# Optimization experiments

Measured on AMD Instinct MI355X. Metric: run time of the kernel, lower is better.

The kernel has to match this reference:

```python
import jax, jax.numpy as jnp
import numpy as np

K = 12           # boundary_k
TEMP = 0.75      # logit_temperature


def _knn_idx(p):
    # p: [N,3]; brute-force kNN within one batch element (pointops offsets => per-batch)
    sq = jnp.sum(p * p, axis=-1)
    d2 = sq[:, None] + sq[None, :] - 2.0 * (p @ p.T)   # [N,N]
    _, idx = jax.lax.top_k(-d2, K + 1)                  # self is nearest (d=0)
    return idx[:, 1:]                                    # drop self -> [N,K]


def _mlp2(x, W1, b1, W2, b2, relu_out):
    h = jax.nn.relu(x @ W1 + b1) @ W2 + b2
    return jax.nn.relu(h) if relu_out else h


def setup_inputs() -> dict:
    key = jax.random.key(0)
    ks = jax.random.split(key, 32)
    B, N, C = 4, 4096, 17
    dims = [256, 512, 768]
    RD = 320
    s = 0.02
    inp = {
        'feat0': jax.random.normal(ks[0], (B, N, dims[0]), jnp.float32),
        'feat1': jax.random.normal(ks[1], (B, N, dims[1]), jnp.float32),
        'feat2': jax.random.normal(ks[2], (B, N, dims[2]), jnp.float32),
        'logits': jax.random.normal(ks[3], (B, N, C), jnp.float32),
        'labels': jax.random.randint(ks[4], (B, N), 0, C, jnp.int32),
        'pos': jax.random.normal(ks[5], (B, N, 3), jnp.float32),
    }
    # feat projections
    for i, d in enumerate(dims):
        inp[f'Wp{i}'] = jax.random.normal(ks[6 + i], (d, RD), jnp.float32) * s
        inp[f'bp{i}'] = jnp.zeros((RD,), jnp.float32)
    # boundary encoder 6->96->160
    inp['Wbe1'] = jax.random.normal(ks[10], (6, 96), jnp.float32) * s
    inp['bbe1'] = jnp.zeros((96,), jnp.float32)
    inp['Wbe2'] = jax.random.normal(ks[11], (96, 160), jnp.float32) * s
    inp['bbe2'] = jnp.zeros((160,), jnp.float32)
    # attention (RD+160)->320->n_scales
    inp['Wa1'] = jax.random.normal(ks[12], (RD + 160, 320), jnp.float32) * s
    inp['ba1'] = jnp.zeros((320,), jnp.float32)
    inp['Wa2'] = jax.random.normal(ks[13], (320, 3), jnp.float32) * s
    inp['ba2'] = jnp.zeros((3,), jnp.float32)
    # output proj RD->RD->RD
    inp['Wo1'] = jax.random.normal(ks[14], (RD, RD), jnp.float32) * s
    inp['bo1'] = jnp.zeros((RD,), jnp.float32)
    inp['Wo2'] = jax.random.normal(ks[15], (RD, RD), jnp.float32) * s
    inp['bo2'] = jnp.zeros((RD,), jnp.float32)
    return inp


def boundary_info(logits, labels, pos):
    idx = jax.vmap(_knn_idx)(pos)                          # [B,N,K]
    nb_lab = jax.vmap(lambda l, i: l[i])(labels, idx)      # [B,N,K]
    nb_pos = jax.vmap(lambda p, i: p[i])(pos, idx)         # [B,N,K,3]
    diff = nb_lab != labels[..., None]                     # [B,N,K]
    diff_f = diff.astype(jnp.float32)
    dist = jnp.linalg.norm(nb_pos - pos[:, :, None, :], axis=-1)  # [B,N,K]
    boundary_score = diff_f.mean(axis=-1)
    same = 1.0 - diff_f
    same_dist = (dist * same).sum(-1) / (same.sum(-1) + 1e-6)
    bdist = jnp.min(jnp.where(diff, dist, jnp.inf), axis=-1)
    bdist = jnp.where(jnp.isfinite(bdist), bdist, same_dist)
    mean_d = dist.mean(-1)
    density = 1.0 / (mean_d + 1e-6)
    curvature = jnp.std(dist, axis=-1, ddof=1) / (mean_d + 1e-6)  # torch.std unbiased
    probs = jax.nn.softmax(logits / TEMP, axis=-1)
    confidence = probs.max(-1)
    entropy = -(probs * jnp.log(probs + 1e-8)).sum(-1) / jnp.log(jnp.float32(probs.shape[-1]))
    return jnp.stack([boundary_score, confidence, entropy, density, curvature, bdist], axis=-1)


def reference(feat0, feat1, feat2, logits, labels, pos,
              Wp0, bp0, Wp1, bp1, Wp2, bp2,
              Wbe1, bbe1, Wbe2, bbe2,
              Wa1, ba1, Wa2, ba2,
              Wo1, bo1, Wo2, bo2):
    fp = jnp.stack([feat0 @ Wp0 + bp0, feat1 @ Wp1 + bp1, feat2 @ Wp2 + bp2], axis=2)  # [B,N,3,RD]
    info = boundary_info(logits, labels, pos)                       # [B,N,6]
    enc = _mlp2(info, Wbe1, bbe1, Wbe2, bbe2, relu_out=True)        # [B,N,160]
    global_feat = fp.mean(axis=2)                                   # [B,N,RD]
    attn_in = jnp.concatenate([global_feat, enc], axis=-1)
    attn = jax.nn.softmax(_mlp2(attn_in, Wa1, ba1, Wa2, ba2, relu_out=False), axis=-1)  # [B,N,3]
    fused = (fp * attn[..., None]).sum(axis=2)                      # [B,N,RD]
    out = _mlp2(fused, Wo1, bo1, Wo2, bo2, relu_out=False) + global_feat
    return out, attn
```

## Files before the change

kernel.cpp:

```cpp
#include <hip/hip_runtime.h>
#include <stdint.h>

typedef float fx4 __attribute__((ext_vector_type(4)));
typedef short s8 __attribute__((ext_vector_type(8)));
typedef short s4 __attribute__((ext_vector_type(4)));
typedef unsigned int u32;
typedef u32 ux4 __attribute__((ext_vector_type(4)));

#define MTOT 16384
#define NPTS 4096

#define VMCNT6 asm volatile("s_waitcnt vmcnt(6)" ::: "memory")
#define VMCNT4 asm volatile("s_waitcnt vmcnt(4)" ::: "memory")
#define VMCNT0 asm volatile("s_waitcnt vmcnt(0)" ::: "memory")
#define LGKM0  asm volatile("s_waitcnt lgkmcnt(0)" ::: "memory")
#define SBAR   asm volatile("s_barrier" ::: "memory")
#define SCHED0 __builtin_amdgcn_sched_barrier(0)

__device__ __forceinline__ float b2f(short s) {
    return __uint_as_float(((unsigned)(unsigned short)s) << 16);
}
__device__ __forceinline__ short f2b(float f) {
    unsigned u = __float_as_uint(f);
    u += 0x7fffu + ((u >> 16) & 1u);
    return (short)(u >> 16);
}
__device__ __forceinline__ void g2l16(const void* g, void* l) {
    __builtin_amdgcn_global_load_lds(
        (const __attribute__((address_space(1))) unsigned int*)g,
        (__attribute__((address_space(3))) unsigned int*)l, 16, 0, 0);
}
__device__ __forceinline__ void g2l4(const void* g, void* l) {
    __builtin_amdgcn_global_load_lds(
        (const __attribute__((address_space(1))) unsigned int*)g,
        (__attribute__((address_space(3))) unsigned int*)l, 4, 0, 0);
}

struct WTDesc {
    const float* W[8];
    short* Bt[8];
    int K[8];
    int N[8];
    int Kp[8];
    int swz[8];
    int base[9];
};

__global__ __launch_bounds__(256) void wtrans8_kernel(WTDesc d)
{
    int idx = blockIdx.x * 256 + threadIdx.x;
    if (idx >= d.base[8]) return;
    int s = 0;
#pragma unroll
    for (int t = 1; t < 8; ++t) if (idx >= d.base[t]) s = t;
    int local = idx - d.base[s];
    int N = d.N[s];
    if (d.swz[s]) {
        int c = local / 10240, r = local - c * 10240;
        int n = r >> 5, q = r & 31, slot = q >> 3, t = q & 7;
        int kl = ((slot ^ ((n >> 1) & 3)) << 3) | t;
        int k = c * 32 + kl;
        d.Bt[s][local] = f2b(d.W[s][(size_t)k * N + n]);
    } else {
        int Kp = d.Kp[s], K = d.K[s];
        int n = local / Kp, k = local - n * Kp;
        d.Bt[s][local] = (k < K) ? f2b(d.W[s][(size_t)k * N + n]) : (short)0;
    }
}

#define SEGW 132
#define KCAP 40

__global__ __launch_bounds__(512) void knap_kernel(
    const float* __restrict__ pos, u32* __restrict__ keys,
    const float* __restrict__ f0, const float* __restrict__ f1, const float* __restrict__ f2,
    short* __restrict__ a0, short* __restrict__ a1, short* __restrict__ a2)
{
    __shared__ float xs[8 * SEGW], ys[8 * SEGW], zs[8 * SEGW];
    __shared__ u32 cand[64 * KCAP];
    __shared__ u32 samp[64 * 16];
    __shared__ u32 tauA[64];
    __shared__ int cnt[64];

    if (blockIdx.x >= 1024) {
        int g = (blockIdx.x - 1024) * 512 + threadIdx.x;
        const float* src; short* dst; int K; size_t w;
        if (g < 1572864)      { src = f2; dst = a2; K = 768; w = (size_t)g * 8; }
        else if (g < 2621440) { src = f1; dst = a1; K = 512; w = (size_t)(g - 1572864) * 8; }
        else                  { src = f0; dst = a0; K = 256; w = (size_t)(g - 2621440) * 8; }
        int Kt = K * 64;
        int mtile = (int)(w / (size_t)Kt);
        int r2 = (int)(w - (size_t)mtile * Kt);
        int chunk = r2 >> 11;
        int within = r2 & 2047;
        int r = within >> 5, q = within & 31;
        int slot = q >> 3;
        int k = chunk * 32 + ((slot ^ ((r >> 1) & 3)) << 3);
        int row = mtile * 64 + r;
        const float* sp = src + (size_t)row * K + k;
        fx4 v0 = *(const fx4*)sp, v1 = *(const fx4*)(sp + 4);
        s8 o;
        o[0] = f2b(v0[0]); o[1] = f2b(v0[1]); o[2] = f2b(v0[2]); o[3] = f2b(v0[3]);
        o[4] = f2b(v1[0]); o[5] = f2b(v1[1]); o[6] = f2b(v1[2]); o[7] = f2b(v1[3]);
        *(s8*)(dst + w) = o;
        return;
    }

    int bid = blockIdx.x;
    int b   = bid >> 8;
    int cc  = (bid >> 6) & 3;
    int pch = bid & 63;
    int tid = threadIdx.x;
    int jb  = cc << 10;

    if (tid < 64) cnt[tid] = 0;
    for (int idx = tid; idx < 1024; idx += 512) {
        int seg = idx >> 7, o = idx & 127;
        const float* pp = pos + (size_t)(b * NPTS + jb + idx) * 3;
        xs[seg * SEGW + o] = pp[0];
        ys[seg * SEGW + o] = pp[1];
        zs[seg * SEGW + o] = pp[2];
    }
    __syncthreads();

    int lp = tid >> 3, q = tid & 7;
    int gi = pch * 64 + lp;
    const float* mp = pos + (size_t)(b * NPTS + gi) * 3;
    float mx = mp[0], my = mp[1], mz = mp[2];

    const float* xsq = xs + q * SEGW;
    const float* ysq = ys + q * SEGW;
    const float* zsq = zs + q * SEGW;
    int jg0 = jb + q * 128;

    u32 h0 = 0xFFFFFFFFu, h1v = 0xFFFFFFFFu;
    for (int jj = 0; jj < 128; jj += 4) {
        fx4 xv = *reinterpret_cast<const fx4*>(xsq + jj);
        fx4 yv = *reinterpret_cast<const fx4*>(ysq + jj);
        fx4 zv = *reinterpret_cast<const fx4*>(zsq + jj);
#pragma unroll
        for (int u = 0; u < 4; ++u) {
            float dx = xv[u] - mx, dy = yv[u] - my, dz = zv[u] - mz;
            float d2 = fmaf(dx, dx, fmaf(dy, dy, dz * dz));
            int jg = jg0 + jj + u;
            u32 key = (__float_as_uint(d2) & 0xFFFFF000u) | (u32)jg;
            if (jg == gi) key = 0xFFFFFFFFu;
            u32 lo = (key < h0) ? key : h0;
            u32 hi = (key < h0) ? h0 : key;
            h0 = lo;
            h1v = (hi < h1v) ? hi : h1v;
        }
    }
    samp[lp * 16 + q * 2]     = h0;
    samp[lp * 16 + q * 2 + 1] = h1v;
    __syncthreads();

    {
        ux4 sv0 = *(ux4*)&samp[lp * 16];
        ux4 sv1 = *(ux4*)&samp[lp * 16 + 4];
        ux4 sv2 = *(ux4*)&samp[lp * 16 + 8];
        ux4 sv3 = *(ux4*)&samp[lp * 16 + 12];
        int r0 = 0, r1 = 0;
#pragma unroll
        for (int i = 0; i < 4; ++i) {
            r0 += (sv0[i] < h0) + (sv1[i] < h0) + (sv2[i] < h0) + (sv3[i] < h0);
            r1 += (sv0[i] < h1v) + (sv1[i] < h1v) + (sv2[i] < h1v) + (sv3[i] < h1v);
        }
        if (r0 == 11) tauA[lp] = h0;
        if (r1 == 11) tauA[lp] = h1v;
    }
    __syncthreads();
    u32 tau = tauA[lp];

    for (int jj = 0; jj < 128; jj += 4) {
        fx4 xv = *reinterpret_cast<const fx4*>(xsq + jj);
        fx4 yv = *reinterpret_cast<const fx4*>(ysq + jj);
        fx4 zv = *reinterpret_cast<const fx4*>(zsq + jj);
#pragma unroll
        for (int u = 0; u < 4; ++u) {
            float dx = xv[u] - mx, dy = yv[u] - my, dz = zv[u] - mz;
            float d2 = fmaf(dx, dx, fmaf(dy, dy, dz * dz));
            int jg = jg0 + jj + u;
            u32 key = (__float_as_uint(d2) & 0xFFFFF000u) | (u32)jg;
            if (jg == gi) key = 0xFFFFFFFFu;
            if (key <= tau) {
                int slot = atomicAdd(&cnt[lp], 1);
                if (slot < KCAP) cand[lp * KCAP + slot] = key;
            }
        }
    }
    __syncthreads();

    int n = cnt[lp];
    u32 out[12];
    if (n <= KCAP) {
        u32 e0, e1, e2, e3, e4;
        e0 = (q      < n) ? cand[lp * KCAP + q]      : 0xFFFFFFFFu;
        e1 = (q + 8  < n) ? cand[lp * KCAP + q + 8]  : 0xFFFFFFFFu;
        e2 = (q + 16 < n) ? cand[lp * KCAP + q + 16] : 0xFFFFFFFFu;
        e3 = (q + 24 < n) ? cand[lp * KCAP + q + 24] : 0xFFFFFFFFu;
        e4 = (q + 32 < n) ? cand[lp * KCAP + q + 32] : 0xFFFFFFFFu;
#define CE(a, b) { u32 t0 = (a < b) ? a : b; u32 t1 = (a < b) ? b : a; a = t0; b = t1; }
        CE(e0, e1) CE(e1, e2) CE(e2, e3) CE(e3, e4)
        CE(e0, e1) CE(e1, e2) CE(e2, e3)
        CE(e0, e1) CE(e1, e2)
        CE(e0, e1)
#undef CE
        cand[lp * KCAP + q]      = e0;
        cand[lp * KCAP + q + 8]  = e1;
        cand[lp * KCAP + q + 16] = e2;
        cand[lp * KCAP + q + 24] = e3;
        cand[lp * KCAP + q + 32] = e4;
        int ptr = 0;
        u32 head = e0;
#pragma unroll
        for (int r = 0; r < 12; ++r) {
            u32 m = head;
            u32 o1 = __shfl_xor(m, 4, 8); m = (o1 < m) ? o1 : m;
            u32 o2 = __shfl_xor(m, 2, 8); m = (o2 < m) ? o2 : m;
            u32 o3 = __shfl_xor(m, 1, 8); m = (o3 < m) ? o3 : m;
            if (m == head) {
                ++ptr;
                head = (ptr < 5) ? cand[lp * KCAP + q + ptr * 8] : 0xFFFFFFFFu;
            }
            out[r] = m;
        }
    } else {
        u32 hk[12];
#pragma unroll
        for (int k = 0; k < 12; ++k) hk[k] = 0xFFFFFFFFu;
        for (int jj = 0; jj < 128; jj += 4) {
            fx4 xv = *reinterpret_cast<const fx4*>(xsq + jj);
            fx4 yv = *reinterpret_cast<const fx4*>(ysq + jj);
            fx4 zv = *reinterpret_cast<const fx4*>(zsq + jj);
#pragma unroll
            for (int u = 0; u < 4; ++u) {
                float dx = xv[u] - mx, dy = yv[u] - my, dz = zv[u] - mz;
                float d2 = fmaf(dx, dx, fmaf(dy, dy, dz * dz));
                int jg = jg0 + jj + u;
                u32 key = (__float_as_uint(d2) & 0xFFFFF000u) | (u32)jg;
                if (jg == gi) key = 0xFFFFFFFFu;
                if (key < hk[11]) {
                    hk[11] = key;
#pragma unroll
                    for (int k = 11; k >= 1; --k) {
                        u32 a = hk[k], bb = hk[k - 1];
                        u32 mn = (a < bb) ? a : bb;
                        u32 mxv = (a < bb) ? bb : a;
                        hk[k - 1] = mn; hk[k] = mxv;
                    }
                }
            }
        }
#pragma unroll
        for (int r = 0; r < 12; ++r) {
            u32 m = hk[0];
            u32 o1 = __shfl_xor(m, 4, 8); m = (o1 < m) ? o1 : m;
            u32 o2 = __shfl_xor(m, 2, 8); m = (o2 < m) ? o2 : m;
            u32 o3 = __shfl_xor(m, 1, 8); m = (o3 < m) ? o3 : m;
            if (m == hk[0]) {
#pragma unroll
                for (int k = 0; k < 11; ++k) hk[k] = hk[k + 1];
                hk[11] = 0xFFFFFFFFu;
            }
            out[r] = m;
        }
    }

    size_t kb = ((size_t)(b * NPTS + gi) * 4 + cc) * 12;
    if (q == 0) *reinterpret_cast<ux4*>(&keys[kb])     = (ux4){out[0], out[1], out[2], out[3]};
    if (q == 1) *reinterpret_cast<ux4*>(&keys[kb + 4]) = (ux4){out[4], out[5], out[6], out[7]};
    if (q == 2) *reinterpret_cast<ux4*>(&keys[kb + 8]) = (ux4){out[8], out[9], out[10], out[11]};
}

__global__ __launch_bounds__(256) void knn_merge_kernel(
    const u32* __restrict__ keys, const int* __restrict__ labels,
    const float* __restrict__ logits, float* __restrict__ info32)
{
    __shared__ unsigned char labs[NPTS];
    int b  = blockIdx.x >> 6;
    int pc = blockIdx.x & 63;
    int tid = threadIdx.x;
    for (int idx = tid; idx < NPTS; idx += 256)
        labs[idx] = (unsigned char)labels[b * NPTS + idx];
    __syncthreads();

    int lp = tid >> 2, q = tid & 3;
    int gi = pc * 64 + lp;
    size_t kb = ((size_t)(b * NPTS + gi) * 4 + q) * 12;
    ux4 k0 = *reinterpret_cast<const ux4*>(&keys[kb]);
    ux4 k1 = *reinterpret_cast<const ux4*>(&keys[kb + 4]);
    ux4 k2 = *reinterpret_cast<const ux4*>(&keys[kb + 8]);
    u32 hk[12];
    hk[0] = k0[0]; hk[1] = k0[1]; hk[2] = k0[2]; hk[3] = k0[3];
    hk[4] = k1[0]; hk[5] = k1[1]; hk[6] = k1[2]; hk[7] = k1[3];
    hk[8] = k2[0]; hk[9] = k2[1]; hk[10] = k2[2]; hk[11] = k2[3];

    int mylab = (int)labs[gi];
    float sum_d = 0.f, sum_d2 = 0.f, sum_diff = 0.f, same_d = 0.f, bmin = 3.0e38f;
#pragma unroll
    for (int r = 0; r < 12; ++r) {
        u32 m = hk[0];
        u32 o1 = __shfl_xor(m, 2, 4); m = (o1 < m) ? o1 : m;
        u32 o2 = __shfl_xor(m, 1, 4); m = (o2 < m) ? o2 : m;
        if (m == hk[0]) {
#pragma unroll
            for (int k = 0; k < 11; ++k) hk[k] = hk[k + 1];
            hk[11] = 0xFFFFFFFFu;
        }
        float d = sqrtf(__uint_as_float(m & 0xFFFFF000u));
        int j = (int)(m & 0xFFFu);
        float isdiff = ((int)labs[j] != mylab) ? 1.0f : 0.0f;
        sum_d += d;
        sum_d2 = fmaf(d, d, sum_d2);
        sum_diff += isdiff;
        same_d = fmaf(d, 1.0f - isdiff, same_d);
        if (isdiff > 0.f) bmin = fminf(bmin, d);
    }

    if (q == 0) {
        float nsame = 12.0f - sum_diff;
        float mean_d = sum_d * (1.0f / 12.0f);
        float var = fmaxf(0.f, (sum_d2 - 12.0f * mean_d * mean_d) * (1.0f / 11.0f));
        float md_eps = mean_d + 1e-6f;
        float curvature = sqrtf(var) / md_eps;
        float density = 1.0f / md_eps;
        float same_dist = same_d / (nsame + 1e-6f);
        float bdist = (bmin < 2.9e38f) ? bmin : same_dist;
        float bscore = sum_diff * (1.0f / 12.0f);

        const float* lg = logits + (size_t)(b * NPTS + gi) * 17;
        float v[17];
        float vmax = -3.0e38f;
#pragma unroll
        for (int c = 0; c < 17; ++c) { v[c] = lg[c] * (1.0f / 0.75f); vmax = fmaxf(vmax, v[c]); }
        float ssum = 0.f;
#pragma unroll
        for (int c = 0; c < 17; ++c) { v[c] = expf(v[c] - vmax); ssum += v[c]; }
        float inv = 1.0f / ssum;
        float conf = 0.f, ent = 0.f;
#pragma unroll
        for (int c = 0; c < 17; ++c) {
            float pprob = v[c] * inv;
            conf = fmaxf(conf, pprob);
            ent += pprob * logf(pprob + 1e-8f);
        }
        ent = -ent * (1.0f / 2.8332133f);

        float* op = info32 + (size_t)(b * NPTS + gi) * 32;
        fx4 o0 = {bscore, conf, ent, density};
        fx4 o1v = {curvature, bdist, 0.f, 0.f};
        fx4 zz = {0.f, 0.f, 0.f, 0.f};
        *reinterpret_cast<fx4*>(op + 0)  = o0;
        *reinterpret_cast<fx4*>(op + 4)  = o1v;
        *reinterpret_cast<fx4*>(op + 8)  = zz;
        *reinterpret_cast<fx4*>(op + 12) = zz;
        *reinterpret_cast<fx4*>(op + 16) = zz;
        *reinterpret_cast<fx4*>(op + 20) = zz;
        *reinterpret_cast<fx4*>(op + 24) = zz;
        *reinterpret_cast<fx4*>(op + 28) = zz;
    }
}

template<bool AF32, bool RELU, bool NMASK, bool ADDF, bool OUTF, bool OUTB>
__global__ __launch_bounds__(256) void gemm_k(
    const void* __restrict__ Ap, int lda,
    const short* __restrict__ Bt,
    const float* __restrict__ bias,
    float* __restrict__ Cf, int ldcf,
    short* __restrict__ Cb, int ldcb, int cboff,
    const float* __restrict__ Af, int ldaf,
    int N, int K, int ntiles)
{
    __shared__ short As[128 * 40];
    __shared__ short Bs[64 * 40];
    int bid = blockIdx.x;
    int mt = bid / ntiles, nt = bid - mt * ntiles;
    int m0 = mt * 128, n0 = nt * 64;
    int tid = threadIdx.x, l = tid & 63, wid = tid >> 6;
    int wm = wid & 1, wn = wid >> 1, lr = l & 15, lh = l >> 4;
    fx4 acc[4][2] = {};

    int nsteps = K >> 5;
    for (int kt = 0; kt < nsteps; ++kt) {
        int k0 = kt << 5;
        if constexpr (AF32) {
            const float* A = (const float*)Ap;
#pragma unroll
            for (int it = 0; it < 4; ++it) {
                int tt = tid + it * 256;
                int row = tt >> 3, seg = tt & 7;
                fx4 vv = *reinterpret_cast<const fx4*>(A + (size_t)(m0 + row) * lda + k0 + seg * 4);
                s4 w; w[0] = f2b(vv[0]); w[1] = f2b(vv[1]); w[2] = f2b(vv[2]); w[3] = f2b(vv[3]);
                *reinterpret_cast<s4*>(&As[row * 40 + seg * 4]) = w;
            }
        } else {
            const short* A = (const short*)Ap;
#pragma unroll
            for (int it = 0; it < 2; ++it) {
                int tt = tid + it * 256;
                int row = tt >> 2, seg = tt & 3;
                s8 vv = *reinterpret_cast<const s8*>(A + (size_t)(m0 + row) * lda + k0 + seg * 8);
                *reinterpret_cast<s8*>(&As[row * 40 + seg * 8]) = vv;
            }
        }
        {
            int row = tid >> 2, seg = tid & 3;
            s8 vb = {0, 0, 0, 0, 0, 0, 0, 0};
            if (!NMASK || (n0 + row) < N)
                vb = *reinterpret_cast<const s8*>(Bt + (size_t)(n0 + row) * K + k0 + seg * 8);
            *reinterpret_cast<s8*>(&Bs[row * 40 + seg * 8]) = vb;
        }
        __syncthreads();
        s8 af[4], bfr[2];
#pragma unroll
        for (int mf = 0; mf < 4; ++mf)
            af[mf] = *reinterpret_cast<s8*>(&As[(wm * 64 + mf * 16 + lr) * 40 + lh * 8]);
#pragma unroll
        for (int nf = 0; nf < 2; ++nf)
            bfr[nf] = *reinterpret_cast<s8*>(&Bs[(wn * 32 + nf * 16 + lr) * 40 + lh * 8]);
#pragma unroll
        for (int mf = 0; mf < 4; ++mf)
#pragma unroll
            for (int nf = 0; nf < 2; ++nf)
                acc[mf][nf] = __builtin_amdgcn_mfma_f32_16x16x32_bf16(af[mf], bfr[nf], acc[mf][nf], 0, 0, 0);
        __syncthreads();
    }

#pragma unroll
    for (int nf = 0; nf < 2; ++nf) {
        int col = n0 + wn * 32 + nf * 16 + lr;
        if (NMASK && col >= N) continue;
        float bv = bias[col];
#pragma unroll
        for (int mf = 0; mf < 4; ++mf) {
            int r0 = m0 + wm * 64 + mf * 16 + lh * 4;
#pragma unroll
            for (int rg = 0; rg < 4; ++rg) {
                float c = acc[mf][nf][rg] + bv;
                if (RELU) c = fmaxf(c, 0.0f);
                int row = r0 + rg;
                if constexpr (ADDF) c += Af[(size_t)row * ldaf + col];
                if constexpr (OUTF) Cf[(size_t)row * ldcf + col] = c;
                if constexpr (OUTB) Cb[(size_t)row * ldcb + cboff + col] = f2b(c);
            }
        }
    }
}

__global__ __launch_bounds__(512, 1) void mega_kernel(
    const short* __restrict__ at0, const short* __restrict__ at1, const short* __restrict__ at2,
    const short* __restrict__ btp0, const short* __restrict__ btp1, const short* __restrict__ btp2,
    const float* __restrict__ bp0, const float* __restrict__ bp1, const float* __restrict__ bp2,
    const short* __restrict__ bta1, const float* __restrict__ ba1,
    const float* __restrict__ Wa2, const float* __restrict__ ba2,
    const short* __restrict__ bto1, const float* __restrict__ bo1,
    const short* __restrict__ bto2, const float* __restrict__ bo2,
    const short* __restrict__ encb,
    float* __restrict__ outf, float* __restrict__ attn_out)
{
    __shared__ alignas(16) char smb[136192];
    const int BBo[3] = {0, 20480, 40960};
    const int ABo[3] = {61440, 65536, 69632};
    constexpr int R2B = 73728, SWF = 135168;
    float* smf = (float*)(smb + SWF);

    int tid = threadIdx.x, wid = tid >> 6, l = tid & 63;
    int wm = wid >> 2, wn = wid & 3, lr = l & 15, lh = l >> 4;
    int m0 = blockIdx.x * 64;

    auto stageB = [&](int bbase, const short* btg, int kt) {
        const char* s = (const char*)(btg + (size_t)kt * 10240);
        int o1 = wid * 1024 + l * 16;
        int o2 = 8192 + o1;
        int o3 = 16384 + wid * 256 + l * 4;
        int o4 = 2048 + o3;
        g2l16(s + o1, smb + bbase + o1);
        g2l16(s + o2, smb + bbase + o2);
        g2l4(s + o3, smb + bbase + o3);
        g2l4(s + o4, smb + bbase + o4);
    };
    auto stageA = [&](int abase, const short* atgm, int kt) {
        const char* s = (const char*)(atgm + (size_t)kt * 2048);
        int o1 = wid * 256 + l * 4;
        int o2 = 2048 + o1;
        g2l4(s + o1, smb + abase + o1);
        g2l4(s + o2, smb + abase + o2);
    };
    auto readB = [&](int bbase, s8* bf) {
#pragma unroll
        for (int nf = 0; nf < 5; ++nf) {
            int row = wn * 80 + nf * 16 + lr;
            bf[nf] = *(const s8*)(smb + bbase + row * 64 + ((lh ^ ((row >> 1) & 3)) << 4));
        }
    };
    auto readA = [&](int abase, s8* af) {
#pragma unroll
        for (int mf = 0; mf < 2; ++mf) {
            int row = wm * 32 + mf * 16 + lr;
            af[mf] = *(const s8*)(smb + abase + row * 64 + ((lh ^ ((row >> 1) & 3)) << 4));
        }
    };

    fx4 gacc[2][5] = {};

    auto do_proj = [&](const short* atgm, const short* btg, int ns,
                       const float* bias, s4 (&fpks)[2][5]) {
        fx4 acc[2][5] = {};
        stageB(BBo[0], btg, 0); stageA(ABo[0], atgm, 0);
        stageB(BBo[1], btg, 1); stageA(ABo[1], atgm, 1);
        LGKM0;
#pragma unroll 1
        for (int kt = 0; kt < ns; ++kt) {
            if (kt < ns - 1) { VMCNT6; } else { VMCNT0; }
            SBAR;
            int ph = kt - (kt / 3) * 3;
            s8 af[2], bf[5];
            readA(ABo[ph], af);
            readB(BBo[ph], bf);
            if (kt + 2 < ns) {
                int p2 = (kt + 2) - ((kt + 2) / 3) * 3;
                stageB(BBo[p2], btg, kt + 2);
                stageA(ABo[p2], atgm, kt + 2);
            }
#pragma unroll
            for (int mf = 0; mf < 2; ++mf)
#pragma unroll
                for (int nf = 0; nf < 5; ++nf)
                    acc[mf][nf] = __builtin_amdgcn_mfma_f32_16x16x32_bf16(af[mf], bf[nf], acc[mf][nf], 0, 0, 0);
            SCHED0; LGKM0;
        }
        SBAR;
#pragma unroll
        for (int nf = 0; nf < 5; ++nf) {
            float bv = bias[wn * 80 + nf * 16 + lr];
#pragma unroll
            for (int mf = 0; mf < 2; ++mf) {
                s4 pk;
#pragma unroll
                for (int rg = 0; rg < 4; ++rg) {
                    float c = acc[mf][nf][rg] + bv;
                    gacc[mf][nf][rg] += c;
                    pk[rg] = f2b(c);
                }
                fpks[mf][nf] = pk;
            }
        }
    };

    s4 fpk0[2][5], fpk1[2][5], fpk2[2][5];
    do_proj(at2 + (size_t)blockIdx.x * 49152, btp2, 24, bp2, fpk2);
    do_proj(at1 + (size_t)blockIdx.x * 32768, btp1, 16, bp1, fpk1);
    do_proj(at0 + (size_t)blockIdx.x * 16384, btp0, 8,  bp0, fpk0);

    s4 gh[2][5];
#pragma unroll
    for (int nf = 0; nf < 5; ++nf) {
        int col = wn * 80 + nf * 16 + lr;
#pragma unroll
        for (int mf = 0; mf < 2; ++mf) {
            s4 pk;
#pragma unroll
            for (int rg = 0; rg < 4; ++rg) {
                int row = wm * 32 + mf * 16 + lh * 4 + rg;
                short gs = f2b(gacc[mf][nf][rg] * (1.0f / 3.0f));
                pk[rg] = gs;
                int bir = (col * 2) ^ (((row >> 1) & 3) << 4);
                *(short*)(smb + R2B + row * 960 + bir) = gs;
            }
            gh[mf][nf] = pk;
        }
    }
#pragma unroll
    for (int r = 0; r < 3; ++r) {
        int idx = tid + r * 512;
        if (idx < 1280) {
            int row = idx / 20, sg = idx - row * 20;
            s8 v = *reinterpret_cast<const s8*>(encb + (size_t)(m0 + row) * 160 + sg * 8);
            int bir = (640 + sg * 16) ^ (((row >> 1) & 3) << 4);
            *(s8*)(smb + R2B + row * 960 + bir) = v;
        }
    }

    auto do_gemm2 = [&](const short* btg, int ns, fx4 (&acc)[2][5]) {
        stageB(BBo[0], btg, 0);
        stageB(BBo[1], btg, 1);
        LGKM0;
#pragma unroll 1
        for (int kt = 0; kt < ns; ++kt) {
            if (kt < ns - 1) { VMCNT4; } else { VMCNT0; }
            SBAR;
            int ph = kt - (kt / 3) * 3;
            s8 af[2], bf[5];
#pragma unroll
            for (int mf = 0; mf < 2; ++mf) {
                int row = wm * 32 + mf * 16 + lr;
                int bir = (kt * 64 + (lh << 4)) ^ (((row >> 1) & 3) << 4);
                af[mf] = *(const s8*)(smb + R2B + row * 960 + bir);
            }
            readB(BBo[ph], bf);
            if (kt + 2 < ns) {
                int p2 = (kt + 2) - ((kt + 2) / 3) * 3;
                stageB(BBo[p2], btg, kt + 2);
            }
#pragma unroll
            for (int mf = 0; mf < 2; ++mf)
#pragma unroll
                for (int nf = 0; nf < 5; ++nf)
                    acc[mf][nf] = __builtin_amdgcn_mfma_f32_16x16x32_bf16(af[mf], bf[nf], acc[mf][nf], 0, 0, 0);
            SCHED0; LGKM0;
        }
        SBAR;
    };

    {
        fx4 acc1[2][5] = {};
        do_gemm2(bta1, 15, acc1);
#pragma unroll
        for (int nf = 0; nf < 5; ++nf) {
            int col = wn * 80 + nf * 16 + lr;
            float bv = ba1[col];
#pragma unroll
            for (int mf = 0; mf < 2; ++mf)
#pragma unroll
                for (int rg = 0; rg < 4; ++rg) {
                    int row = wm * 32 + mf * 16 + lh * 4 + rg;
                    int bir = (col * 2) ^ (((row >> 1) & 3) << 4);
                    *(short*)(smb + R2B + row * 960 + bir) = f2b(fmaxf(acc1[mf][nf][rg] + bv, 0.0f));
                }
        }
    }

    {
        float* ws2 = (float*)smb;
        if (tid < 240)
            reinterpret_cast<fx4*>(ws2)[tid] = reinterpret_cast<const fx4*>(Wa2)[tid];
        __syncthreads();
        int row = tid >> 3, g = tid & 7;
        float l0 = 0.f, l1 = 0.f, l2 = 0.f;
#pragma unroll
        for (int j = 0; j < 5; ++j) {
            int bir = (g * 80 + j * 16) ^ (((row >> 1) & 3) << 4);
            s8 v = *(const s8*)(smb + R2B + row * 960 + bir);
#pragma unroll
            for (int u = 0; u < 8; ++u) {
                float f = b2f(v[u]);
                const float* wp = ws2 + (g * 40 + j * 8 + u) * 3;
                l0 = fmaf(f, wp[0], l0);
                l1 = fmaf(f, wp[1], l1);
                l2 = fmaf(f, wp[2], l2);
            }
        }
#pragma unroll
        for (int s = 4; s >= 1; s >>= 1) {
            l0 += __shfl_xor(l0, s, 8);
            l1 += __shfl_xor(l1, s, 8);
            l2 += __shfl_xor(l2, s, 8);
        }
        if (g == 0) {
            l0 += ba2[0]; l1 += ba2[1]; l2 += ba2[2];
            float mx = fmaxf(l0, fmaxf(l1, l2));
            float e0 = expf(l0 - mx), e1 = expf(l1 - mx), e2 = expf(l2 - mx);
            float inv = 1.0f / (e0 + e1 + e2);
            float w0 = e0 * inv, w1 = e1 * inv, w2 = e2 * inv;
            attn_out[(size_t)(m0 + row) * 3 + 0] = w0;
            attn_out[(size_t)(m0 + row) * 3 + 1] = w1;
            attn_out[(size_t)(m0 + row) * 3 + 2] = w2;
            smf[row * 4 + 0] = w0; smf[row * 4 + 1] = w1; smf[row * 4 + 2] = w2;
        }
        __syncthreads();
    }

#pragma unroll
    for (int mf = 0; mf < 2; ++mf)
#pragma unroll
        for (int rg = 0; rg < 4; ++rg) {
            int row = wm * 32 + mf * 16 + lh * 4 + rg;
            float w0 = smf[row * 4 + 0], w1 = smf[row * 4 + 1], w2 = smf[row * 4 + 2];
#pragma unroll
            for (int nf = 0; nf < 5; ++nf) {
                int col = wn * 80 + nf * 16 + lr;
                float fv = w0 * b2f(fpk0[mf][nf][rg])
                         + w1 * b2f(fpk1[mf][nf][rg])
                         + w2 * b2f(fpk2[mf][nf][rg]);
                int bir = (col * 2) ^ (((row >> 1) & 3) << 4);
                *(short*)(smb + R2B + row * 960 + bir) = f2b(fv);
            }
        }

    {
        fx4 acch[2][5] = {};
        do_gemm2(bto1, 10, acch);
#pragma unroll
        for (int nf = 0; nf < 5; ++nf) {
            int col = wn * 80 + nf * 16 + lr;
            float bv = bo1[col];
#pragma unroll
            for (int mf = 0; mf < 2; ++mf)
#pragma unroll
                for (int rg = 0; rg < 4; ++rg) {
                    int row = wm * 32 + mf * 16 + lh * 4 + rg;
                    int bir = (col * 2) ^ (((row >> 1) & 3) << 4);
                    *(short*)(smb + R2B + row * 960 + bir) = f2b(fmaxf(acch[mf][nf][rg] + bv, 0.0f));
                }
        }
    }

    {
        fx4 acco[2][5] = {};
        do_gemm2(bto2, 10, acco);
#pragma unroll
        for (int nf = 0; nf < 5; ++nf) {
            int col = wn * 80 + nf * 16 + lr;
            float bv = bo2[col];
#pragma unroll
            for (int mf = 0; mf < 2; ++mf)
#pragma unroll
                for (int rg = 0; rg < 4; ++rg) {
                    int row = m0 + wm * 32 + mf * 16 + lh * 4 + rg;
                    float c = acco[mf][nf][rg] + bv + b2f(gh[mf][nf][rg]);
                    outf[(size_t)row * 320 + col] = c;
                }
        }
    }
}

extern "C" void kernel_launch(void* const* d_in, const int* in_sizes, int n_in,
                              void* d_out, int out_size, void* d_ws, size_t ws_size,
                              hipStream_t stream)
{
    const float* feat0  = (const float*)d_in[0];
    const float* feat1  = (const float*)d_in[1];
    const float* feat2  = (const float*)d_in[2];
    const float* logits = (const float*)d_in[3];
    const int*   labels = (const int*)d_in[4];
    const float* pos    = (const float*)d_in[5];
    const float* Wp0 = (const float*)d_in[6];   const float* bp0 = (const float*)d_in[7];
    const float* Wp1 = (const float*)d_in[8];   const float* bp1 = (const float*)d_in[9];
    const float* Wp2 = (const float*)d_in[10];  const float* bp2 = (const float*)d_in[11];
    const float* Wbe1 = (const float*)d_in[12]; const float* bbe1 = (const float*)d_in[13];
    const float* Wbe2 = (const float*)d_in[14]; const float* bbe2 = (const float*)d_in[15];
    const float* Wa1 = (const float*)d_in[16];  const float* ba1 = (const float*)d_in[17];
    const float* Wa2 = (const float*)d_in[18];  const float* ba2 = (const float*)d_in[19];
    const float* Wo1 = (const float*)d_in[20];  const float* bo1 = (const float*)d_in[21];
    const float* Wo2 = (const float*)d_in[22];  const float* bo2 = (const float*)d_in[23];

    char* p = (char*)d_ws;
    auto alloc = [&](size_t bytes) { char* r = p; p += (bytes + 255) & ~(size_t)255; return r; };
    short* bt_p0  = (short*)alloc((size_t)320 * 256 * 2);
    short* bt_p1  = (short*)alloc((size_t)320 * 512 * 2);
    short* bt_p2  = (short*)alloc((size_t)320 * 768 * 2);
    short* bt_be1 = (short*)alloc((size_t)96 * 32 * 2);
    short* bt_be2 = (short*)alloc((size_t)160 * 96 * 2);
    short* bt_a1  = (short*)alloc((size_t)320 * 480 * 2);
    short* bt_o1  = (short*)alloc((size_t)320 * 320 * 2);
    short* bt_o2  = (short*)alloc((size_t)320 * 320 * 2);
    float* info32 = (float*)alloc((size_t)MTOT * 32 * 4);
    short* h1     = (short*)alloc((size_t)MTOT * 96 * 2);
    short* encb   = (short*)alloc((size_t)MTOT * 160 * 2);
    u32*   knnkeys= (u32*)alloc((size_t)MTOT * 4 * 12 * 4);
    short* abt0   = (short*)alloc((size_t)MTOT * 256 * 2);
    short* abt1   = (short*)alloc((size_t)MTOT * 512 * 2);
    short* abt2   = (short*)alloc((size_t)MTOT * 768 * 2);

    float* outf = (float*)d_out;
    float* attn_out = outf + (size_t)MTOT * 320;

    WTDesc wd;
    const float* Ws[8] = {Wp0, Wp1, Wp2, Wbe1, Wbe2, Wa1, Wo1, Wo2};
    short* Bts[8] = {bt_p0, bt_p1, bt_p2, bt_be1, bt_be2, bt_a1, bt_o1, bt_o2};
    int Ks[8]  = {256, 512, 768, 6, 96, 480, 320, 320};
    int Ns[8]  = {320, 320, 320, 96, 160, 320, 320, 320};
    int Kps[8] = {256, 512, 768, 32, 96, 480, 320, 320};
    int Sz[8]  = {1, 1, 1, 0, 0, 1, 1, 1};
    int acc = 0;
    for (int s = 0; s < 8; ++s) {
        wd.W[s] = Ws[s]; wd.Bt[s] = Bts[s];
        wd.K[s] = Ks[s]; wd.N[s] = Ns[s]; wd.Kp[s] = Kps[s]; wd.swz[s] = Sz[s];
        wd.base[s] = acc;
        acc += Ns[s] * Kps[s];
    }
    wd.base[8] = acc;
    wtrans8_kernel<<<(acc + 255) / 256, 256, 0, stream>>>(wd);

    knap_kernel<<<7168, 512, 0, stream>>>(pos, knnkeys,
                                          feat0, feat1, feat2,
                                          abt0, abt1, abt2);
    knn_merge_kernel<<<256, 256, 0, stream>>>(knnkeys, labels, logits, info32);

    gemm_k<true, true, true, false, false, true><<<256, 256, 0, stream>>>(
        info32, 32, bt_be1, bbe1, nullptr, 0, h1, 96, 0, nullptr, 0, 96, 32, 2);
    gemm_k<false, true, true, false, false, true><<<384, 256, 0, stream>>>(
        h1, 96, bt_be2, bbe2, nullptr, 0, encb, 160, 0, nullptr, 0, 160, 96, 3);

    mega_kernel<<<256, 512, 0, stream>>>(
        abt0, abt1, abt2,
        bt_p0, bt_p1, bt_p2,
        bp0, bp1, bp2,
        bt_a1, ba1, Wa2, ba2,
        bt_o1, bo1, bt_o2, bo2,
        encb, outf, attn_out);
}
```

Baseline: 156.7 us.

## Recompute the three projection GEMMs after attention instead of holding them in registers

Instead of keeping the three bf16-packed per-scale projection tiles live in registers across the attention stage, the kernel now runs the projections twice. The first pass accumulates only their sum, used for the global mean. After the attention weights are computed, a second pass redoes each projection and folds it into an fp32 fused accumulator with fmaf. This cuts register pressure, which could raise occupancy or remove spills, and keeps the fused value in fp32 rather than rounding each scale to bf16. The cost is doubling the projection MFMA work and re-streaming the large feature inputs from global memory.

```diff
diff --git a/kernel.cpp b/kernel.cpp
--- a/kernel.cpp
+++ b/kernel.cpp
@@ -502,11 +502,7 @@
         }
     };
 
-    fx4 gacc[2][5] = {};
-
-    auto do_proj = [&](const short* atgm, const short* btg, int ns,
-                       const float* bias, s4 (&fpks)[2][5]) {
-        fx4 acc[2][5] = {};
+    auto do_projacc = [&](const short* atgm, const short* btg, int ns, fx4 (&acc)[2][5]) {
         stageB(BBo[0], btg, 0); stageA(ABo[0], atgm, 0);
         stageB(BBo[1], btg, 1); stageA(ABo[1], atgm, 1);
         LGKM0;
@@ -531,39 +527,29 @@
             SCHED0; LGKM0;
         }
         SBAR;
-#pragma unroll
-        for (int nf = 0; nf < 5; ++nf) {
-            float bv = bias[wn * 80 + nf * 16 + lr];
-#pragma unroll
-            for (int mf = 0; mf < 2; ++mf) {
-                s4 pk;
-#pragma unroll
-                for (int rg = 0; rg < 4; ++rg) {
-                    float c = acc[mf][nf][rg] + bv;
-                    gacc[mf][nf][rg] += c;
-                    pk[rg] = f2b(c);
-                }
-                fpks[mf][nf] = pk;
-            }
-        }
     };
 
-    s4 fpk0[2][5], fpk1[2][5], fpk2[2][5];
-    do_proj(at2 + (size_t)blockIdx.x * 49152, btp2, 24, bp2, fpk2);
-    do_proj(at1 + (size_t)blockIdx.x * 32768, btp1, 16, bp1, fpk1);
-    do_proj(at0 + (size_t)blockIdx.x * 16384, btp0, 8,  bp0, fpk0);
+    const short* at2m = at2 + (size_t)blockIdx.x * 49152;
+    const short* at1m = at1 + (size_t)blockIdx.x * 32768;
+    const short* at0m = at0 + (size_t)blockIdx.x * 16384;
+
+    fx4 gsum[2][5] = {};
+    do_projacc(at2m, btp2, 24, gsum);
+    do_projacc(at1m, btp1, 16, gsum);
+    do_projacc(at0m, btp0, 8,  gsum);
 
     s4 gh[2][5];
 #pragma unroll
     for (int nf = 0; nf < 5; ++nf) {
         int col = wn * 80 + nf * 16 + lr;
+        float bsum = bp0[col] + bp1[col] + bp2[col];
 #pragma unroll
         for (int mf = 0; mf < 2; ++mf) {
             s4 pk;
 #pragma unroll
             for (int rg = 0; rg < 4; ++rg) {
                 int row = wm * 32 + mf * 16 + lh * 4 + rg;
-                short gs = f2b(gacc[mf][nf][rg] * (1.0f / 3.0f));
+                short gs = f2b((gsum[mf][nf][rg] + bsum) * (1.0f / 3.0f));
                 pk[rg] = gs;
                 int bir = (col * 2) ^ (((row >> 1) & 3) << 4);
                 *(short*)(smb + R2B + row * 960 + bir) = gs;
@@ -671,22 +657,65 @@
         __syncthreads();
     }
 
-#pragma unroll
-    for (int mf = 0; mf < 2; ++mf)
-#pragma unroll
-        for (int rg = 0; rg < 4; ++rg) {
-            int row = wm * 32 + mf * 16 + lh * 4 + rg;
-            float w0 = smf[row * 4 + 0], w1 = smf[row * 4 + 1], w2 = smf[row * 4 + 2];
-#pragma unroll
-            for (int nf = 0; nf < 5; ++nf) {
-                int col = wn * 80 + nf * 16 + lr;
-                float fv = w0 * b2f(fpk0[mf][nf][rg])
-                         + w1 * b2f(fpk1[mf][nf][rg])
-                         + w2 * b2f(fpk2[mf][nf][rg]);
+    fx4 fused[2][5] = {};
+    {
+        fx4 acc2[2][5] = {};
+        do_projacc(at2m, btp2, 24, acc2);
+#pragma unroll
+        for (int nf = 0; nf < 5; ++nf) {
+            float bv = bp2[wn * 80 + nf * 16 + lr];
+#pragma unroll
+            for (int mf = 0; mf < 2; ++mf)
+#pragma unroll
+                for (int rg = 0; rg < 4; ++rg) {
+                    int row = wm * 32 + mf * 16 + lh * 4 + rg;
+                    fused[mf][nf][rg] = fmaf(smf[row * 4 + 2], acc2[mf][nf][rg] + bv, fused[mf][nf][rg]);
+                }
+        }
+    }
+    {
+        fx4 acc2[2][5] = {};
+        do_projacc(at1m, btp1, 16, acc2);
+#pragma unroll
+        for (int nf = 0; nf < 5; ++nf) {
+            float bv = bp1[wn * 80 + nf * 16 + lr];
+#pragma unroll
+            for (int mf = 0; mf < 2; ++mf)
+#pragma unroll
+                for (int rg = 0; rg < 4; ++rg) {
+                    int row = wm * 32 + mf * 16 + lh * 4 + rg;
+                    fused[mf][nf][rg] = fmaf(smf[row * 4 + 1], acc2[mf][nf][rg] + bv, fused[mf][nf][rg]);
+                }
+        }
+    }
+    {
+        fx4 acc2[2][5] = {};
+        do_projacc(at0m, btp0, 8, acc2);
+#pragma unroll
+        for (int nf = 0; nf < 5; ++nf) {
+            float bv = bp0[wn * 80 + nf * 16 + lr];
+#pragma unroll
+            for (int mf = 0; mf < 2; ++mf)
+#pragma unroll
+                for (int rg = 0; rg < 4; ++rg) {
+                    int row = wm * 32 + mf * 16 + lh * 4 + rg;
+                    fused[mf][nf][rg] = fmaf(smf[row * 4 + 0], acc2[mf][nf][rg] + bv, fused[mf][nf][rg]);
+                }
+        }
+    }
+
+#pragma unroll
+    for (int nf = 0; nf < 5; ++nf) {
+        int col = wn * 80 + nf * 16 + lr;
+#pragma unroll
+        for (int mf = 0; mf < 2; ++mf)
+#pragma unroll
+            for (int rg = 0; rg < 4; ++rg) {
+                int row = wm * 32 + mf * 16 + lh * 4 + rg;
                 int bir = (col * 2) ^ (((row >> 1) & 3) << 4);
-                *(short*)(smb + R2B + row * 960 + bir) = f2b(fv);
-            }
-        }
+                *(short*)(smb + R2B + row * 960 + bir) = f2b(fused[mf][nf][rg]);
+            }
+    }
 
     {
         fx4 acch[2][5] = {};
```

Result: slower. 171.0 us (+9.1%).

## Double mega_kernel block to 1024 threads with one M-fragment per wave

Applied to the files above, without the earlier changes.

Launches the fused projection/attention/output kernel with 1024 threads (16 waves) per block instead of 512, giving each wave a single 16-row M fragment instead of two. Staging loads are redistributed so each thread issues fewer global-to-LDS copies, and the vmcnt waits are reduced to match. This aims to raise latency hiding and per-CU wave parallelism, but it halves the MFMA work per wave per barrier, so A-operand reuse drops and barrier overhead rises relative to compute.

```diff
diff --git a/kernel.cpp b/kernel.cpp
--- a/kernel.cpp
+++ b/kernel.cpp
@@ -10,8 +10,8 @@
 #define MTOT 16384
 #define NPTS 4096
 
-#define VMCNT6 asm volatile("s_waitcnt vmcnt(6)" ::: "memory")
-#define VMCNT4 asm volatile("s_waitcnt vmcnt(4)" ::: "memory")
+#define VMCNT3 asm volatile("s_waitcnt vmcnt(3)" ::: "memory")
+#define VMCNT2 asm volatile("s_waitcnt vmcnt(2)" ::: "memory")
 #define VMCNT0 asm volatile("s_waitcnt vmcnt(0)" ::: "memory")
 #define LGKM0  asm volatile("s_waitcnt lgkmcnt(0)" ::: "memory")
 #define SBAR   asm volatile("s_barrier" ::: "memory")
@@ -448,7 +448,7 @@
     }
 }
 
-__global__ __launch_bounds__(512, 1) void mega_kernel(
+__global__ __launch_bounds__(1024, 1) void mega_kernel(
     const short* __restrict__ at0, const short* __restrict__ at1, const short* __restrict__ at2,
     const short* __restrict__ btp0, const short* __restrict__ btp1, const short* __restrict__ btp2,
     const float* __restrict__ bp0, const float* __restrict__ bp1, const float* __restrict__ bp2,
@@ -471,21 +471,14 @@
 
     auto stageB = [&](int bbase, const short* btg, int kt) {
         const char* s = (const char*)(btg + (size_t)kt * 10240);
-        int o1 = wid * 1024 + l * 16;
-        int o2 = 8192 + o1;
-        int o3 = 16384 + wid * 256 + l * 4;
-        int o4 = 2048 + o3;
+        int o1 = tid * 16;
+        int o2 = 16384 + tid * 4;
         g2l16(s + o1, smb + bbase + o1);
-        g2l16(s + o2, smb + bbase + o2);
-        g2l4(s + o3, smb + bbase + o3);
-        g2l4(s + o4, smb + bbase + o4);
+        g2l4(s + o2, smb + bbase + o2);
     };
     auto stageA = [&](int abase, const short* atgm, int kt) {
         const char* s = (const char*)(atgm + (size_t)kt * 2048);
-        int o1 = wid * 256 + l * 4;
-        int o2 = 2048 + o1;
-        g2l4(s + o1, smb + abase + o1);
-        g2l4(s + o2, smb + abase + o2);
+        g2l4(s + tid * 4, smb + abase + tid * 4);
     };
     auto readB = [&](int bbase, s8* bf) {
 #pragma unroll
@@ -494,29 +487,25 @@
             bf[nf] = *(const s8*)(smb + bbase + row * 64 + ((lh ^ ((row >> 1) & 3)) << 4));
         }
     };
-    auto readA = [&](int abase, s8* af) {
-#pragma unroll
-        for (int mf = 0; mf < 2; ++mf) {
-            int row = wm * 32 + mf * 16 + lr;
-            af[mf] = *(const s8*)(smb + abase + row * 64 + ((lh ^ ((row >> 1) & 3)) << 4));
-        }
-    };
-
-    fx4 gacc[2][5] = {};
+
+    fx4 gacc[5] = {};
 
     auto do_proj = [&](const short* atgm, const short* btg, int ns,
-                       const float* bias, s4 (&fpks)[2][5]) {
-        fx4 acc[2][5] = {};
+                       const float* bias, s4 (&fpks)[5]) {
+        fx4 acc[5] = {};
         stageB(BBo[0], btg, 0); stageA(ABo[0], atgm, 0);
         stageB(BBo[1], btg, 1); stageA(ABo[1], atgm, 1);
         LGKM0;
 #pragma unroll 1
         for (int kt = 0; kt < ns; ++kt) {
-            if (kt < ns - 1) { VMCNT6; } else { VMCNT0; }
+            if (kt < ns - 1) { VMCNT3; } else { VMCNT0; }
             SBAR;
             int ph = kt - (kt / 3) * 3;
-            s8 af[2], bf[5];
-            readA(ABo[ph], af);
+            s8 af, bf[5];
+            {
+                int row = wm * 16 + lr;
+                af = *(const s8*)(smb + ABo[ph] + row * 64 + ((lh ^ ((row >> 1) & 3)) << 4));
+            }
             readB(BBo[ph], bf);
             if (kt + 2 < ns) {
                 int p2 = (kt + 2) - ((kt + 2) / 3) * 3;
@@ -524,56 +513,48 @@
                 stageA(ABo[p2], atgm, kt + 2);
             }
 #pragma unroll
-            for (int mf = 0; mf < 2; ++mf)
-#pragma unroll
-                for (int nf = 0; nf < 5; ++nf)
-                    acc[mf][nf] = __builtin_amdgcn_mfma_f32_16x16x32_bf16(af[mf], bf[nf], acc[mf][nf], 0, 0, 0);
+            for (int nf = 0; nf < 5; ++nf)
+                acc[nf] = __builtin_amdgcn_mfma_f32_16x16x32_bf16(af, bf[nf], acc[nf], 0, 0, 0);
             SCHED0; LGKM0;
         }
         SBAR;
 #pragma unroll
         for (int nf = 0; nf < 5; ++nf) {
             float bv = bias[wn * 80 + nf * 16 + lr];
-#pragma unroll
-            for (int mf = 0; mf < 2; ++mf) {
-                s4 pk;
-#pragma unroll
-                for (int rg = 0; rg < 4; ++rg) {
-                    float c = acc[mf][nf][rg] + bv;
-                    gacc[mf][nf][rg] += c;
-                    pk[rg] = f2b(c);
-                }
-                fpks[mf][nf] = pk;
-            }
+            s4 pk;
+#pragma unroll
+            for (int rg = 0; rg < 4; ++rg) {
+                float c = acc[nf][rg] + bv;
+                gacc[nf][rg] += c;
+                pk[rg] = f2b(c);
+            }
+            fpks[nf] = pk;
         }
     };
 
-    s4 fpk0[2][5], fpk1[2][5], fpk2[2][5];
+    s4 fpk0[5], fpk1[5], fpk2[5];
     do_proj(at2 + (size_t)blockIdx.x * 49152, btp2, 24, bp2, fpk2);
     do_proj(at1 + (size_t)blockIdx.x * 32768, btp1, 16, bp1, fpk1);
     do_proj(at0 + (size_t)blockIdx.x * 16384, btp0, 8,  bp0, fpk0);
 
-    s4 gh[2][5];
+    s4 gh[5];
 #pragma unroll
     for (int nf = 0; nf < 5; ++nf) {
         int col = wn * 80 + nf * 16 + lr;
-#pragma unroll
-        for (int mf = 0; mf < 2; ++mf) {
-            s4 pk;
-#pragma unroll
-            for (int rg = 0; rg < 4; ++rg) {
-                int row = wm * 32 + mf * 16 + lh * 4 + rg;
-                short gs = f2b(gacc[mf][nf][rg] * (1.0f / 3.0f));
-                pk[rg] = gs;
-                int bir = (col * 2) ^ (((row >> 1) & 3) << 4);
-                *(short*)(smb + R2B + row * 960 + bir) = gs;
-            }
-            gh[mf][nf] = pk;
-        }
-    }
-#pragma unroll
-    for (int r = 0; r < 3; ++r) {
-        int idx = tid + r * 512;
+        s4 pk;
+#pragma unroll
+        for (int rg = 0; rg < 4; ++rg) {
+            int row = wm * 16 + lh * 4 + rg;
+            short gs = f2b(gacc[nf][rg] * (1.0f / 3.0f));
+            pk[rg] = gs;
+            int bir = (col * 2) ^ (((row >> 1) & 3) << 4);
+            *(short*)(smb + R2B + row * 960 + bir) = gs;
+        }
+        gh[nf] = pk;
+    }
+#pragma unroll
+    for (int r = 0; r < 2; ++r) {
+        int idx = tid + r * 1024;
         if (idx < 1280) {
             int row = idx / 20, sg = idx - row * 20;
             s8 v = *reinterpret_cast<const s8*>(encb + (size_t)(m0 + row) * 160 + sg * 8);
@@ -582,21 +563,20 @@
         }
     }
 
-    auto do_gemm2 = [&](const short* btg, int ns, fx4 (&acc)[2][5]) {
+    auto do_gemm2 = [&](const short* btg, int ns, fx4 (&acc)[5]) {
         stageB(BBo[0], btg, 0);
         stageB(BBo[1], btg, 1);
         LGKM0;
 #pragma unroll 1
         for (int kt = 0; kt < ns; ++kt) {
-            if (kt < ns - 1) { VMCNT4; } else { VMCNT0; }
+            if (kt < ns - 1) { VMCNT2; } else { VMCNT0; }
             SBAR;
             int ph = kt - (kt / 3) * 3;
-            s8 af[2], bf[5];
-#pragma unroll
-            for (int mf = 0; mf < 2; ++mf) {
-                int row = wm * 32 + mf * 16 + lr;
+            s8 af, bf[5];
+            {
+                int row = wm * 16 + lr;
                 int bir = (kt * 64 + (lh << 4)) ^ (((row >> 1) & 3) << 4);
-                af[mf] = *(const s8*)(smb + R2B + row * 960 + bir);
+                af = *(const s8*)(smb + R2B + row * 960 + bir);
             }
             readB(BBo[ph], bf);
             if (kt + 2 < ns) {
@@ -604,30 +584,26 @@
                 stageB(BBo[p2], btg, kt + 2);
             }
 #pragma unroll
-            for (int mf = 0; mf < 2; ++mf)
-#pragma unroll
-                for (int nf = 0; nf < 5; ++nf)
-                    acc[mf][nf] = __builtin_amdgcn_mfma_f32_16x16x32_bf16(af[mf], bf[nf], acc[mf][nf], 0, 0, 0);
+            for (int nf = 0; nf < 5; ++nf)
+                acc[nf] = __builtin_amdgcn_mfma_f32_16x16x32_bf16(af, bf[nf], acc[nf], 0, 0, 0);
             SCHED0; LGKM0;
         }
         SBAR;
     };
 
     {
-        fx4 acc1[2][5] = {};
+        fx4 acc1[5] = {};
         do_gemm2(bta1, 15, acc1);
 #pragma unroll
         for (int nf = 0; nf < 5; ++nf) {
             int col = wn * 80 + nf * 16 + lr;
             float bv = ba1[col];
 #pragma unroll
-            for (int mf = 0; mf < 2; ++mf)
-#pragma unroll
-                for (int rg = 0; rg < 4; ++rg) {
-                    int row = wm * 32 + mf * 16 + lh * 4 + rg;
-                    int bir = (col * 2) ^ (((row >> 1) & 3) << 4);
-                    *(short*)(smb + R2B + row * 960 + bir) = f2b(fmaxf(acc1[mf][nf][rg] + bv, 0.0f));
-                }
+            for (int rg = 0; rg < 4; ++rg) {
+                int row = wm * 16 + lh * 4 + rg;
+                int bir = (col * 2) ^ (((row >> 1) & 3) << 4);
+                *(short*)(smb + R2B + row * 960 + bir) = f2b(fmaxf(acc1[nf][rg] + bv, 0.0f));
+            }
         }
     }
 
@@ -636,91 +612,87 @@
         if (tid < 240)
             reinterpret_cast<fx4*>(ws2)[tid] = reinterpret_cast<const fx4*>(Wa2)[tid];
         __syncthreads();
-        int row = tid >> 3, g = tid & 7;
-        float l0 = 0.f, l1 = 0.f, l2 = 0.f;
-#pragma unroll
-        for (int j = 0; j < 5; ++j) {
-            int bir = (g * 80 + j * 16) ^ (((row >> 1) & 3) << 4);
-            s8 v = *(const s8*)(smb + R2B + row * 960 + bir);
-#pragma unroll
-            for (int u = 0; u < 8; ++u) {
-                float f = b2f(v[u]);
-                const float* wp = ws2 + (g * 40 + j * 8 + u) * 3;
-                l0 = fmaf(f, wp[0], l0);
-                l1 = fmaf(f, wp[1], l1);
-                l2 = fmaf(f, wp[2], l2);
-            }
-        }
-#pragma unroll
-        for (int s = 4; s >= 1; s >>= 1) {
-            l0 += __shfl_xor(l0, s, 8);
-            l1 += __shfl_xor(l1, s, 8);
-            l2 += __shfl_xor(l2, s, 8);
-        }
-        if (g == 0) {
-            l0 += ba2[0]; l1 += ba2[1]; l2 += ba2[2];
-            float mx = fmaxf(l0, fmaxf(l1, l2));
-            float e0 = expf(l0 - mx), e1 = expf(l1 - mx), e2 = expf(l2 - mx);
-            float inv = 1.0f / (e0 + e1 + e2);
-            float w0 = e0 * inv, w1 = e1 * inv, w2 = e2 * inv;
-            attn_out[(size_t)(m0 + row) * 3 + 0] = w0;
-            attn_out[(size_t)(m0 + row) * 3 + 1] = w1;
-            attn_out[(size_t)(m0 + row) * 3 + 2] = w2;
-            smf[row * 4 + 0] = w0; smf[row * 4 + 1] = w1; smf[row * 4 + 2] = w2;
+        if (tid < 512) {
+            int row = tid >> 3, g = tid & 7;
+            float l0 = 0.f, l1 = 0.f, l2 = 0.f;
+#pragma unroll
+            for (int j = 0; j < 5; ++j) {
+                int bir = (g * 80 + j * 16) ^ (((row >> 1) & 3) << 4);
+                s8 v = *(const s8*)(smb + R2B + row * 960 + bir);
+#pragma unroll
+                for (int u = 0; u < 8; ++u) {
+                    float f = b2f(v[u]);
+                    const float* wp = ws2 + (g * 40 + j * 8 + u) * 3;
+                    l0 = fmaf(f, wp[0], l0);
+                    l1 = fmaf(f, wp[1], l1);
+                    l2 = fmaf(f, wp[2], l2);
+                }
+            }
+#pragma unroll
+            for (int s = 4; s >= 1; s >>= 1) {
+                l0 += __shfl_xor(l0, s, 8);
+                l1 += __shfl_xor(l1, s, 8);
+                l2 += __shfl_xor(l2, s, 8);
+            }
+            if (g == 0) {
+                l0 += ba2[0]; l1 += ba2[1]; l2 += ba2[2];
+                float mx = fmaxf(l0, fmaxf(l1, l2));
+                float e0 = expf(l0 - mx), e1 = expf(l1 - mx), e2 = expf(l2 - mx);
+                float inv = 1.0f / (e0 + e1 + e2);
+                float w0 = e0 * inv, w1 = e1 * inv, w2 = e2 * inv;
+                attn_out[(size_t)(m0 + row) * 3 + 0] = w0;
+                attn_out[(size_t)(m0 + row) * 3 + 1] = w1;
+                attn_out[(size_t)(m0 + row) * 3 + 2] = w2;
+                smf[row * 4 + 0] = w0; smf[row * 4 + 1] = w1; smf[row * 4 + 2] = w2;
+            }
         }
         __syncthreads();
     }
 
 #pragma unroll
-    for (int mf = 0; mf < 2; ++mf)
-#pragma unroll
-        for (int rg = 0; rg < 4; ++rg) {
-            int row = wm * 32 + mf * 16 + lh * 4 + rg;
-            float w0 = smf[row * 4 + 0], w1 = smf[row * 4 + 1], w2 = smf[row * 4 + 2];
-#pragma unroll
-            for (int nf = 0; nf < 5; ++nf) {
-                int col = wn * 80 + nf * 16 + lr;
-                float fv = w0 * b2f(fpk0[mf][nf][rg])
-                         + w1 * b2f(fpk1[mf][nf][rg])
-                         + w2 * b2f(fpk2[mf][nf][rg]);
-                int bir = (col * 2) ^ (((row >> 1) & 3) << 4);
-                *(short*)(smb + R2B + row * 960 + bir) = f2b(fv);
-            }
-        }
+    for (int rg = 0; rg < 4; ++rg) {
+        int row = wm * 16 + lh * 4 + rg;
+        float w0 = smf[row * 4 + 0], w1 = smf[row * 4 + 1], w2 = smf[row * 4 + 2];
+#pragma unroll
+        for (int nf = 0; nf < 5; ++nf) {
+            int col = wn * 80 + nf * 16 + lr;
+            float fv = w0 * b2f(fpk0[nf][rg])
+                     + w1 * b2f(fpk1[nf][rg])
+                     + w2 * b2f(fpk2[nf][rg]);
+            int bir = (col * 2) ^ (((row >> 1) & 3) << 4);
+            *(short*)(smb + R2B + row * 960 + bir) = f2b(fv);
+        }
+    }
 
     {
-        fx4 acch[2][5] = {};
+        fx4 acch[5] = {};
         do_gemm2(bto1, 10, acch);
 #pragma unroll
         for (int nf = 0; nf < 5; ++nf) {
             int col = wn * 80 + nf * 16 + lr;
             float bv = bo1[col];
 #pragma unroll
-            for (int mf = 0; mf < 2; ++mf)
-#pragma unroll
-                for (int rg = 0; rg < 4; ++rg) {
-                    int row = wm * 32 + mf * 16 + lh * 4 + rg;
-                    int bir = (col * 2) ^ (((row >> 1) & 3) << 4);
-                    *(short*)(smb + R2B + row * 960 + bir) = f2b(fmaxf(acch[mf][nf][rg] + bv, 0.0f));
-                }
+            for (int rg = 0; rg < 4; ++rg) {
+                int row = wm * 16 + lh * 4 + rg;
+                int bir = (col * 2) ^ (((row >> 1) & 3) << 4);
+                *(short*)(smb + R2B + row * 960 + bir) = f2b(fmaxf(acch[nf][rg] + bv, 0.0f));
+            }
         }
     }
 
     {
-        fx4 acco[2][5] = {};
+        fx4 acco[5] = {};
         do_gemm2(bto2, 10, acco);
 #pragma unroll
         for (int nf = 0; nf < 5; ++nf) {
             int col = wn * 80 + nf * 16 + lr;
             float bv = bo2[col];
 #pragma unroll
-            for (int mf = 0; mf < 2; ++mf)
-#pragma unroll
-                for (int rg = 0; rg < 4; ++rg) {
-                    int row = m0 + wm * 32 + mf * 16 + lh * 4 + rg;
-                    float c = acco[mf][nf][rg] + bv + b2f(gh[mf][nf][rg]);
-                    outf[(size_t)row * 320 + col] = c;
-                }
+            for (int rg = 0; rg < 4; ++rg) {
+                int row = m0 + wm * 16 + lh * 4 + rg;
+                float c = acco[nf][rg] + bv + b2f(gh[nf][rg]);
+                outf[(size_t)row * 320 + col] = c;
+            }
         }
     }
 }
@@ -793,7 +765,7 @@
     gemm_k<false, true, true, false, false, true><<<384, 256, 0, stream>>>(
         h1, 96, bt_be2, bbe2, nullptr, 0, encb, 160, 0, nullptr, 0, 160, 96, 3);
 
-    mega_kernel<<<256, 512, 0, stream>>>(
+    mega_kernel<<<256, 1024, 0, stream>>>(
         abt0, abt1, abt2,
         bt_p0, bt_p1, bt_p2,
         bp0, bp1, bp2,
```

New measurement: 158.1 us. No clear change (+0.9%).
